# Kernel optimization log

Measured on AMD Instinct MI355X. Metric: run time of the kernel, lower is better.

The kernel has to match this reference:

```python
import jax, jax.numpy as jnp
import numpy as np

B, S_LEN, H, NH, NT, NL, I = 8, 2048, 768, 12, 32, 9, 3072
SPAN = 64
NSP = S_LEN // SPAN
TAG_RATE = 2
DH = H // NH
EPS = 1e-12


def rope(x):
    # interleaved-pair rotary position embedding, x: [B, L, H]
    L = x.shape[1]
    half = x.shape[2] // 2
    inv = 1.0 / (10000.0 ** (jnp.arange(half, dtype=jnp.float32) / half))
    ang = jnp.arange(L, dtype=jnp.float32)[:, None] * inv[None, :]  # [L, half]
    sin, cos = jnp.sin(ang), jnp.cos(ang)
    x2 = x.reshape(x.shape[0], L, half, 2)
    xe, xo = x2[..., 0], x2[..., 1]
    return jnp.stack([xe * cos - xo * sin, xe * sin + xo * cos], axis=-1).reshape(x.shape)


def layernorm(x, g, b):
    m = jnp.mean(x, axis=-1, keepdims=True)
    v = jnp.mean((x - m) ** 2, axis=-1, keepdims=True)
    return (x - m) * jax.lax.rsqrt(v + EPS) * g + b


def mha(q_in, kv_in, Wqkv, bqkv, Wo, bo):
    # torch nn.MultiheadAttention math (eval), batched over leading span axis
    Wq, Wk, Wv = jnp.split(Wqkv, 3, axis=0)
    bq, bk, bv = jnp.split(bqkv, 3)
    def heads(x, W, b):
        return (x @ W.T + b).reshape(x.shape[0], x.shape[1], NH, DH)
    q = heads(q_in, Wq, bq)
    k = heads(kv_in, Wk, bk)
    v = heads(kv_in, Wv, bv)
    scores = jnp.einsum('nqhd,nkhd->nhqk', q, k) * (1.0 / DH ** 0.5)
    a = jax.nn.softmax(scores, axis=-1)
    o = jnp.einsum('nhqk,nkhd->nqhd', a, v).reshape(q_in.shape[0], q_in.shape[1], H)
    return o @ Wo.T + bo


def setup_inputs() -> dict:
    key = jax.random.key(0)
    ks = jax.random.split(key, 16)
    p = lambda i, shape: (0.02 * jax.random.normal(ks[i], shape)).astype(jnp.float32)
    inp = {}
    inp['word_embedding'] = jax.random.normal(ks[0], (B, S_LEN, H), dtype=jnp.float32)
    # fixed-length, non-overlapping spans covering the sequence
    inp['span_starts'] = jnp.broadcast_to(jnp.arange(NSP, dtype=jnp.int32) * SPAN, (B, NSP))
    inp['span_tags'] = jax.random.randint(ks[1], (B, NSP), 0, NT)
    inp['tag_emb'] = p(2, (NT, H))
    inp['sa_Wqkv'] = p(3, (3 * H, H)); inp['sa_bqkv'] = jnp.zeros((3 * H,), jnp.float32)
    inp['sa_Wo'] = p(4, (H, H)); inp['sa_bo'] = jnp.zeros((H,), jnp.float32)
    inp['at_Wqkv'] = p(5, (3 * H, H)); inp['at_bqkv'] = jnp.zeros((3 * H,), jnp.float32)
    inp['at_Wo'] = p(6, (H, H)); inp['at_bo'] = jnp.zeros((H,), jnp.float32)
    inp['an_g'] = jnp.ones((H,), jnp.float32); inp['an_b'] = jnp.zeros((H,), jnp.float32)
    inp['W1'] = p(7, (I, H)); inp['b1'] = jnp.zeros((I,), jnp.float32)
    inp['W2'] = p(8, (H, I)); inp['b2'] = jnp.zeros((H,), jnp.float32)
    inp['fn_g'] = jnp.ones((H,), jnp.float32); inp['fn_b'] = jnp.zeros((H,), jnp.float32)
    inp['Wout'] = p(9, (NL, H)); inp['bout'] = jnp.zeros((NL,), jnp.float32)
    return inp


def reference(word_embedding, span_starts, span_tags, tag_emb,
              sa_Wqkv, sa_bqkv, sa_Wo, sa_bo,
              at_Wqkv, at_bqkv, at_Wo, at_bo,
              an_g, an_b, W1, b1, W2, b2, fn_g, fn_b, Wout, bout):
    raw = word_embedding  # hidden dropout p=0 (eval) -> identity
    xe = rope(word_embedding)
    # pack all spans: [B, NSP*SPAN] token positions
    pos = (span_starts[..., None] + jnp.arange(SPAN)).reshape(B, NSP * SPAN)
    spans = jnp.take_along_axis(xe, pos[..., None], axis=1).reshape(B * NSP, SPAN, H)
    # if_add_a_self_attention: X += self_attention(X, X, X)
    X = spans + mha(spans, spans, sa_Wqkv, sa_bqkv, sa_Wo, sa_bo)
    # enumerate_mode == 'self_attention': prepend tag embedding token, self-attend, drop it
    tagv = tag_emb[span_tags.reshape(-1)][:, None, :]  # [B*NSP, 1, H]
    qkv = jnp.concatenate([tagv, X], axis=1)           # [B*NSP, SPAN+1, H]
    res = mha(qkv, qkv, at_Wqkv, at_bqkv, at_Wo, at_bo)[:, 1:, :]
    # scatter-add results back into the full sequence
    taged = jnp.zeros_like(word_embedding).at[jnp.arange(B)[:, None], pos].add(
        res.reshape(B, NSP * SPAN, H))
    # if_merge_by_add branch
    out_emb = layernorm(raw + taged * TAG_RATE, an_g, an_b)
    ff = jax.nn.relu(out_emb @ W1.T + b1) @ W2.T + b2
    out = layernorm(ff + out_emb, fn_g, fn_b)
    return out @ Wout.T + bout
```

## Files before the change

kernel.cpp:

```cpp
#include <hip/hip_runtime.h>


typedef __attribute__((ext_vector_type(8))) short short8;
typedef __attribute__((ext_vector_type(4))) float f32x4;

typedef const __attribute__((address_space(1))) unsigned int* gas1_t;
typedef __attribute__((address_space(3))) unsigned int* las3_t;

#define DEVI static __device__ __forceinline__

DEVI void gload_lds16(const void* g, void* l){
  __builtin_amdgcn_global_load_lds((gas1_t)g, (las3_t)l, 16, 0, 0);
}

template<int N> DEVI void vmcnt_imm(){
  if constexpr (N == 8) asm volatile("s_waitcnt vmcnt(8)" ::: "memory");
  else if constexpr (N == 4) asm volatile("s_waitcnt vmcnt(4)" ::: "memory");
  else asm volatile("s_waitcnt vmcnt(0)" ::: "memory");
}

DEVI unsigned short f2bf(float f){
  union { float f; unsigned u; } v; v.f = f;
  unsigned u = v.u;
  return (unsigned short)((u + 0x7fffu + ((u >> 16) & 1u)) >> 16);
}
DEVI float bf2f(unsigned short h){
  union { unsigned u; float f; } v; v.u = ((unsigned)h) << 16; return v.f;
}

__global__ void k_ropetab(float2* __restrict__ tab){
  int idx = blockIdx.x * 256 + threadIdx.x;
  if (idx >= 2048 * 384) return;
  int l = idx / 384, i = idx % 384;
  float inv = __expf(-(float)i * (9.210340371976184f / 384.0f));
  float ang = (float)l * inv;
  tab[idx] = make_float2(cosf(ang), sinf(ang));
}

__global__ void k_f2bf_all(const float* __restrict__ s0, const float* __restrict__ s1,
                           const float* __restrict__ s2, const float* __restrict__ s3,
                           const float* __restrict__ s4, const float* __restrict__ s5,
                           unsigned short* __restrict__ dst){
  int i = blockIdx.x * 256 + threadIdx.x;
  int e = i * 4;
  const float* src; int off;
  if      (e < 1769472){ src = s0; off = e; }
  else if (e < 2359296){ src = s1; off = e - 1769472; }
  else if (e < 4128768){ src = s2; off = e - 2359296; }
  else if (e < 4718592){ src = s3; off = e - 4128768; }
  else if (e < 7077888){ src = s4; off = e - 4718592; }
  else                 { src = s5; off = e - 7077888; }
  float4 v = *(const float4*)(src + off);
  ushort4 o;
  o.x = f2bf(v.x); o.y = f2bf(v.y); o.z = f2bf(v.z); o.w = f2bf(v.w);
  *(ushort4*)(dst + e) = o;
}

__global__ void k_gather_rope(const float* __restrict__ we, const int* __restrict__ starts,
                              const float2* __restrict__ tab, unsigned short* __restrict__ spans){
  int idx = blockIdx.x * 256 + threadIdx.x;
  int r  = idx / 192;
  int c4 = idx % 192;
  int span = r >> 6, s = r & 63;
  int b = span >> 5;
  int l = starts[span] + s;
  float4 x = *(const float4*)(we + ((size_t)b * 2048 + l) * 768 + c4 * 4);
  int i0 = c4 * 2;
  float2 cs0 = tab[l * 384 + i0];
  float2 cs1 = tab[l * 384 + i0 + 1];
  ushort4 o;
  o.x = f2bf(x.x * cs0.x - x.y * cs0.y);
  o.y = f2bf(x.x * cs0.y + x.y * cs0.x);
  o.z = f2bf(x.z * cs1.x - x.w * cs1.y);
  o.w = f2bf(x.z * cs1.y + x.w * cs1.x);
  *(ushort4*)(spans + (size_t)r * 768 + c4 * 4) = o;
}

__global__ void k_fill_tag(const float* __restrict__ tag_emb, const int* __restrict__ tags,
                           unsigned short* __restrict__ at_in){
  int span = blockIdx.x;
  int tag = tags[span];
  const float* src = tag_emb + (size_t)tag * 768;
  unsigned short* dst = at_in + (size_t)span * 65 * 768;
  for (int j = threadIdx.x; j < 768; j += 256) dst[j] = f2bf(src[j]);
}

template<int EPI>
__global__ __launch_bounds__(512, 2)
void k_gemm256(const unsigned short* __restrict__ A, const unsigned short* __restrict__ Bw,
               const float* __restrict__ bias, void* __restrict__ outp,
               const unsigned short* __restrict__ resid, int M, int N, int K, int nbx)
{
  __shared__ unsigned short Asl[4 * 256 * 32];
  __shared__ unsigned short Bsl[4 * 256 * 32];
  const int t0 = threadIdx.x;
  const int w = t0 >> 6, lane = t0 & 63;
  const int g = lane >> 4, li = lane & 15;
  const int wm = w >> 2, wn = w & 3;

  const int nwg = gridDim.x;
  const int bid = blockIdx.x;
  const int q = nwg >> 3, r8 = nwg & 7;
  const int xcd = bid & 7, off = bid >> 3;
  const int swz = (xcd < r8 ? xcd * (q + 1) : r8 * (q + 1) + (xcd - r8) * q) + off;
  int mt, nt;
  const int main_ = nbx << 6;
  if (swz >= main_){ mt = 64; nt = swz - main_; }
  else {
    const int s = swz / 12, wv = swz % 12;
    const int nsc = nbx / 3;
    mt = (s / nsc) * 4 + (wv & 3);
    nt = (s % nsc) * 3 + (wv >> 2);
  }
  const int m0 = mt * 256, n0 = nt * 256;

  const int srow = lane >> 2;
  const int sgc = (((lane & 3) ^ ((lane >> 3) & 3)) << 3);
  const int cs = ((g ^ ((li >> 1) & 3)) << 3);

  f32x4 acc[8][4];
  #pragma unroll
  for (int i = 0; i < 8; i++)
    #pragma unroll
    for (int j = 0; j < 4; j++) acc[i][j] = f32x4{0.f, 0.f, 0.f, 0.f};

  const int KT = K >> 5;

  #define STAGE(t_, s_) do { \
    const unsigned short* ga0 = A  + (size_t)(m0 +       w*16 + srow) * K + (t_)*32 + sgc; \
    const unsigned short* ga1 = A  + (size_t)(m0 + 128 + w*16 + srow) * K + (t_)*32 + sgc; \
    const unsigned short* gb0 = Bw + (size_t)(n0 +       w*16 + srow) * K + (t_)*32 + sgc; \
    const unsigned short* gb1 = Bw + (size_t)(n0 + 128 + w*16 + srow) * K + (t_)*32 + sgc; \
    gload_lds16(ga0, Asl + (s_)*8192 + (      w*16)*32); \
    gload_lds16(ga1, Asl + (s_)*8192 + (128 + w*16)*32); \
    gload_lds16(gb0, Bsl + (s_)*8192 + (      w*16)*32); \
    gload_lds16(gb1, Bsl + (s_)*8192 + (128 + w*16)*32); \
  } while(0)

  STAGE(0, 0);
  STAGE(1, 1);
  STAGE(2, 2);
  vmcnt_imm<8>();
  __builtin_amdgcn_s_barrier();

  for (int t = 0; t < KT; ++t){
    const int slot = t & 3;
    const unsigned short* As = Asl + slot * 8192;
    const unsigned short* Bs = Bsl + slot * 8192;

    short8 af[8], bfr[4];
    #pragma unroll
    for (int m = 0; m < 8; m++)
      af[m] = *(const short8*)(As + (wm * 128 + m * 16 + li) * 32 + cs);
    #pragma unroll
    for (int n = 0; n < 4; n++)
      bfr[n] = *(const short8*)(Bs + (wn * 64 + n * 16 + li) * 32 + cs);

    if (t + 3 < KT) STAGE(t + 3, (t + 3) & 3);

    __builtin_amdgcn_s_setprio(1);
    #pragma unroll
    for (int m = 0; m < 8; m++)
      #pragma unroll
      for (int n = 0; n < 4; n++)
        acc[m][n] = __builtin_amdgcn_mfma_f32_16x16x32_bf16(af[m], bfr[n], acc[m][n], 0, 0, 0);
    __builtin_amdgcn_s_setprio(0);

    if (t + 1 < KT){
      __builtin_amdgcn_sched_barrier(0);
      if (t + 3 < KT)      vmcnt_imm<8>();
      else if (t + 2 < KT) vmcnt_imm<4>();
      else                 vmcnt_imm<0>();
      __builtin_amdgcn_s_barrier();
    }
  }
  #undef STAGE

  unsigned short* outb = (unsigned short*)outp;
  float* outf = (float*)outp;
  #pragma unroll
  for (int m = 0; m < 8; m++){
    const int row = m0 + wm * 128 + m * 16 + g * 4;
    #pragma unroll
    for (int n = 0; n < 4; n++){
      const int col = n0 + wn * 64 + n * 16 + li;
      const float bv = bias[col];
      #pragma unroll
      for (int r = 0; r < 4; r++){
        float v = acc[m][n][r] + bv;
        const int orow = row + r;
        if (EPI == 1) v += bf2f(resid[(size_t)orow * N + col]);
        if (EPI == 3) v = v > 0.f ? v : 0.f;
        if (EPI == 2){
          outf[(size_t)orow * N + col] = v;
        } else if (EPI == 1){
          outb[(size_t)(orow + orow / 64 + 1) * N + col] = f2bf(v);
        } else {
          outb[(size_t)orow * N + col] = f2bf(v);
        }
      }
    }
  }
}

template<int AT>
__global__ __launch_bounds__(64)
void k_attn(const unsigned short* __restrict__ qkv, unsigned short* __restrict__ outp)
{
  constexpr int Lkv  = AT ? 65 : 64;
  constexpr int qoff = AT ? 1 : 0;
  constexpr int NKF  = AT ? 5 : 4;
  constexpr int VK   = AT ? 65 : 64;
  constexpr int KKPV = AT ? 3 : 2;
  const int h = blockIdx.x;
  const int span = blockIdx.y;
  const int base = span * Lkv;
  const int lane = threadIdx.x;
  const int g = lane >> 4, li = lane & 15;

  __shared__ unsigned short P[64 * 104];
  if (AT){
    #pragma unroll
    for (int j = 0; j < 16; j++) P[lane * 104 + 80 + j] = 0;
  }

  short8 qf[4][2];
  #pragma unroll
  for (int m = 0; m < 4; m++)
    #pragma unroll
    for (int kq = 0; kq < 2; kq++)
      qf[m][kq] = *(const short8*)(qkv + (size_t)(base + qoff + m * 16 + li) * 2304 + h * 64 + kq * 32 + g * 8);

  f32x4 sc[4][NKF];
  #pragma unroll
  for (int m = 0; m < 4; m++)
    #pragma unroll
    for (int n = 0; n < NKF; n++) sc[m][n] = f32x4{0.f, 0.f, 0.f, 0.f};

  #pragma unroll
  for (int kq = 0; kq < 2; kq++){
    #pragma unroll
    for (int n = 0; n < NKF; n++){
      int krow = n * 16 + li; if (krow >= Lkv) krow = Lkv - 1;
      short8 kf = *(const short8*)(qkv + (size_t)(base + krow) * 2304 + 768 + h * 64 + kq * 32 + g * 8);
      #pragma unroll
      for (int m = 0; m < 4; m++)
        sc[m][n] = __builtin_amdgcn_mfma_f32_16x16x32_bf16(qf[m][kq], kf, sc[m][n], 0, 0, 0);
    }
  }

  const float scale = 0.125f;
  #pragma unroll
  for (int m = 0; m < 4; m++){
    #pragma unroll
    for (int r = 0; r < 4; r++){
      float mx = -1e30f;
      #pragma unroll
      for (int n = 0; n < NKF; n++){
        float v = sc[m][n][r] * scale;
        if (n * 16 + li >= VK) v = -1e30f;
        sc[m][n][r] = v;
        mx = fmaxf(mx, v);
      }
      mx = fmaxf(mx, __shfl_xor(mx, 1, 64));
      mx = fmaxf(mx, __shfl_xor(mx, 2, 64));
      mx = fmaxf(mx, __shfl_xor(mx, 4, 64));
      mx = fmaxf(mx, __shfl_xor(mx, 8, 64));
      float sum = 0.f;
      #pragma unroll
      for (int n = 0; n < NKF; n++){
        float p = __expf(sc[m][n][r] - mx);
        sc[m][n][r] = p;
        sum += p;
      }
      sum += __shfl_xor(sum, 1, 64);
      sum += __shfl_xor(sum, 2, 64);
      sum += __shfl_xor(sum, 4, 64);
      sum += __shfl_xor(sum, 8, 64);
      const float inv = 1.f / sum;
      const int prow = m * 16 + g * 4 + r;
      #pragma unroll
      for (int n = 0; n < NKF; n++)
        P[prow * 104 + n * 16 + li] = f2bf(sc[m][n][r] * inv);
    }
  }
  __syncthreads();

  f32x4 oacc[4][4];
  #pragma unroll
  for (int m = 0; m < 4; m++)
    #pragma unroll
    for (int n = 0; n < 4; n++) oacc[m][n] = f32x4{0.f, 0.f, 0.f, 0.f};

  #pragma unroll
  for (int kp = 0; kp < KKPV; kp++){
    short8 pf[4];
    #pragma unroll
    for (int m = 0; m < 4; m++)
      pf[m] = *(const short8*)(P + (m * 16 + li) * 104 + kp * 32 + g * 8);
    #pragma unroll
    for (int n = 0; n < 4; n++){
      short8 vf;
      #pragma unroll
      for (int i = 0; i < 8; i++){
        int k = kp * 32 + g * 8 + i;
        unsigned short vv = 0;
        if (k < VK) vv = qkv[(size_t)(base + k) * 2304 + 1536 + h * 64 + n * 16 + li];
        vf[i] = (short)vv;
      }
      #pragma unroll
      for (int m = 0; m < 4; m++)
        oacc[m][n] = __builtin_amdgcn_mfma_f32_16x16x32_bf16(pf[m], vf, oacc[m][n], 0, 0, 0);
    }
  }

  #pragma unroll
  for (int m = 0; m < 4; m++)
    #pragma unroll
    for (int n = 0; n < 4; n++)
      #pragma unroll
      for (int r = 0; r < 4; r++){
        int q = m * 16 + g * 4 + r;
        outp[(size_t)(span * 64 + q) * 768 + h * 64 + n * 16 + li] = f2bf(oacc[m][n][r]);
      }
}

__global__ __launch_bounds__(256)
void k_ln1(const float* __restrict__ raw, const float* __restrict__ res,
           const int* __restrict__ starts, const float* __restrict__ gg,
           const float* __restrict__ bb, unsigned short* __restrict__ oe16)
{
  int wave = threadIdx.x >> 6, lane = threadIdx.x & 63;
  int r = blockIdx.x * 4 + wave;
  int span = r >> 6, s = r & 63;
  int b = span >> 5;
  int l = starts[span] + s;
  const float* rp = raw + ((size_t)b * 2048 + l) * 768;
  const float* qp = res + (size_t)r * 768;
  float x[12];
  float sum = 0.f;
  #pragma unroll
  for (int j = 0; j < 12; j++){
    int c = lane + j * 64;
    x[j] = rp[c] + 2.f * qp[c];
    sum += x[j];
  }
  #pragma unroll
  for (int o = 1; o < 64; o <<= 1) sum += __shfl_xor(sum, o, 64);
  float mean = sum * (1.f / 768.f);
  float vs = 0.f;
  #pragma unroll
  for (int j = 0; j < 12; j++){ float d = x[j] - mean; vs += d * d; }
  #pragma unroll
  for (int o = 1; o < 64; o <<= 1) vs += __shfl_xor(vs, o, 64);
  float rstd = rsqrtf(vs * (1.f / 768.f) + 1e-12f);
  size_t ob = ((size_t)b * 2048 + l) * 768;
  #pragma unroll
  for (int j = 0; j < 12; j++){
    int c = lane + j * 64;
    float y = (x[j] - mean) * rstd * gg[c] + bb[c];
    oe16[ob + c] = f2bf(y);
  }
}

__global__ __launch_bounds__(256)
void k_ln2_out(const unsigned short* __restrict__ ff2, const unsigned short* __restrict__ oe,
               const float* __restrict__ gg, const float* __restrict__ bb,
               const float* __restrict__ Wout, const float* __restrict__ bout,
               float* __restrict__ out)
{
  int wave = threadIdx.x >> 6, lane = threadIdx.x & 63;
  int t = blockIdx.x * 4 + wave;
  const unsigned short* fp = ff2 + (size_t)t * 768;
  const unsigned short* ep = oe  + (size_t)t * 768;
  float x[12];
  float sum = 0.f;
  #pragma unroll
  for (int j = 0; j < 12; j++){
    int c = lane + j * 64;
    x[j] = bf2f(fp[c]) + bf2f(ep[c]);
    sum += x[j];
  }
  #pragma unroll
  for (int o = 1; o < 64; o <<= 1) sum += __shfl_xor(sum, o, 64);
  float mean = sum * (1.f / 768.f);
  float vs = 0.f;
  #pragma unroll
  for (int j = 0; j < 12; j++){ float d = x[j] - mean; vs += d * d; }
  #pragma unroll
  for (int o = 1; o < 64; o <<= 1) vs += __shfl_xor(vs, o, 64);
  float rstd = rsqrtf(vs * (1.f / 768.f) + 1e-12f);
  #pragma unroll
  for (int j = 0; j < 12; j++){
    int c = lane + j * 64;
    x[j] = (x[j] - mean) * rstd * gg[c] + bb[c];
  }
  for (int n = 0; n < 9; n++){
    float p = 0.f;
    #pragma unroll
    for (int j = 0; j < 12; j++){
      int c = lane + j * 64;
      p += x[j] * Wout[n * 768 + c];
    }
    #pragma unroll
    for (int o = 1; o < 64; o <<= 1) p += __shfl_xor(p, o, 64);
    if (lane == 0) out[(size_t)t * 9 + n] = p + bout[n];
  }
}

extern "C" void kernel_launch(void* const* d_in, const int* in_sizes, int n_in,
                              void* d_out, int out_size, void* d_ws, size_t ws_size,
                              hipStream_t stream)
{
  const float* we      = (const float*)d_in[0];
  const int*   starts  = (const int*)d_in[1];
  const int*   tags    = (const int*)d_in[2];
  const float* tag_emb = (const float*)d_in[3];
  const float* sa_Wqkv = (const float*)d_in[4];
  const float* sa_bqkv = (const float*)d_in[5];
  const float* sa_Wo   = (const float*)d_in[6];
  const float* sa_bo   = (const float*)d_in[7];
  const float* at_Wqkv = (const float*)d_in[8];
  const float* at_bqkv = (const float*)d_in[9];
  const float* at_Wo   = (const float*)d_in[10];
  const float* at_bo   = (const float*)d_in[11];
  const float* an_g    = (const float*)d_in[12];
  const float* an_b    = (const float*)d_in[13];
  const float* W1      = (const float*)d_in[14];
  const float* b1      = (const float*)d_in[15];
  const float* W2      = (const float*)d_in[16];
  const float* b2      = (const float*)d_in[17];
  const float* fn_g    = (const float*)d_in[18];
  const float* fn_b    = (const float*)d_in[19];
  const float* Wout    = (const float*)d_in[20];
  const float* bout    = (const float*)d_in[21];
  float* out = (float*)d_out;
  char* ws = (char*)d_ws;

  unsigned short* spans   = (unsigned short*)(ws + 0);
  unsigned short* at_in   = (unsigned short*)(ws + 25165824);
  unsigned short* attno   = (unsigned short*)(ws + 50724864);
  unsigned short* qkv     = (unsigned short*)(ws + 75890688);
  float2*         ropetab = (float2*)(ws + 75890688);
  float*          resf    = (float*)(ws + 75890688);
  unsigned short* oe16    = (unsigned short*)(ws + 0);
  unsigned short* ff1     = (unsigned short*)(ws + 25165824);
  unsigned short* ff2     = (unsigned short*)(ws + 125829120);
  unsigned short* wb      = (unsigned short*)(ws + 152567808);
  unsigned short* sa_Wqkv_b = wb;
  unsigned short* sa_Wo_b   = sa_Wqkv_b + 2304 * 768;
  unsigned short* at_Wqkv_b = sa_Wo_b   + 768 * 768;
  unsigned short* at_Wo_b   = at_Wqkv_b + 2304 * 768;
  unsigned short* W1_b      = at_Wo_b   + 768 * 768;
  unsigned short* W2_b      = W1_b      + 3072 * 768;

  k_ropetab<<<3072, 256, 0, stream>>>(ropetab);
  k_f2bf_all<<<9216, 256, 0, stream>>>(sa_Wqkv, sa_Wo, at_Wqkv, at_Wo, W1, W2, wb);
  k_gather_rope<<<12288, 256, 0, stream>>>(we, starts, ropetab, spans);

  k_gemm256<0><<<576, 512, 0, stream>>>(spans, sa_Wqkv_b, sa_bqkv, qkv, nullptr, 16384, 2304, 768, 9);
  k_attn<0><<<dim3(12, 256), 64, 0, stream>>>(qkv, attno);
  k_fill_tag<<<256, 256, 0, stream>>>(tag_emb, tags, at_in);
  k_gemm256<1><<<192, 512, 0, stream>>>(attno, sa_Wo_b, sa_bo, at_in, spans, 16384, 768, 768, 3);
  k_gemm256<0><<<585, 512, 0, stream>>>(at_in, at_Wqkv_b, at_bqkv, qkv, nullptr, 16640, 2304, 768, 9);
  k_attn<1><<<dim3(12, 256), 64, 0, stream>>>(qkv, attno);
  k_gemm256<2><<<192, 512, 0, stream>>>(attno, at_Wo_b, at_bo, resf, nullptr, 16384, 768, 768, 3);
  k_ln1<<<4096, 256, 0, stream>>>(we, resf, starts, an_g, an_b, oe16);
  k_gemm256<3><<<768, 512, 0, stream>>>(oe16, W1_b, b1, ff1, nullptr, 16384, 3072, 768, 12);
  k_gemm256<0><<<192, 512, 0, stream>>>(ff1, W2_b, b2, ff2, nullptr, 16384, 768, 3072, 3);
  k_ln2_out<<<4096, 256, 0, stream>>>(ff2, oe16, fn_g, fn_b, Wout, bout, out);
}
```

Baseline: 500.0 us.

## Split GEMM k-step into two MFMA halves with interleaved A/B staging

The GEMM main loop is unrolled by four so LDS slots are indexed statically. Each k-step is split into two MFMA phases over the upper and lower halves of the A tile. The global-to-LDS loads for A and B are issued separately, one ahead of each phase, with barriers and priority bumps around every phase. The goal is to overlap loads with MFMA work in a finer-grained, ping-pong-like way and to hold fewer A fragments in registers at once. In exchange it adds four barriers per k-step and assumes K/32 is a multiple of four.

```diff
diff --git a/kernel.cpp b/kernel.cpp
--- a/kernel.cpp
+++ b/kernel.cpp
@@ -126,55 +126,72 @@
 
   const int KT = K >> 5;
 
-  #define STAGE(t_, s_) do { \
+  #define STAGE_A(t_, s_) do { \
     const unsigned short* ga0 = A  + (size_t)(m0 +       w*16 + srow) * K + (t_)*32 + sgc; \
     const unsigned short* ga1 = A  + (size_t)(m0 + 128 + w*16 + srow) * K + (t_)*32 + sgc; \
+    gload_lds16(ga0, Asl + (s_)*8192 + (      w*16)*32); \
+    gload_lds16(ga1, Asl + (s_)*8192 + (128 + w*16)*32); \
+  } while(0)
+  #define STAGE_B(t_, s_) do { \
     const unsigned short* gb0 = Bw + (size_t)(n0 +       w*16 + srow) * K + (t_)*32 + sgc; \
     const unsigned short* gb1 = Bw + (size_t)(n0 + 128 + w*16 + srow) * K + (t_)*32 + sgc; \
-    gload_lds16(ga0, Asl + (s_)*8192 + (      w*16)*32); \
-    gload_lds16(ga1, Asl + (s_)*8192 + (128 + w*16)*32); \
     gload_lds16(gb0, Bsl + (s_)*8192 + (      w*16)*32); \
     gload_lds16(gb1, Bsl + (s_)*8192 + (128 + w*16)*32); \
   } while(0)
 
-  STAGE(0, 0);
-  STAGE(1, 1);
-  STAGE(2, 2);
+  STAGE_A(0, 0); STAGE_B(0, 0);
+  STAGE_A(1, 1); STAGE_B(1, 1);
+  STAGE_A(2, 2); STAGE_B(2, 2);
   vmcnt_imm<8>();
   __builtin_amdgcn_s_barrier();
 
-  for (int t = 0; t < KT; ++t){
-    const int slot = t & 3;
-    const unsigned short* As = Asl + slot * 8192;
-    const unsigned short* Bs = Bsl + slot * 8192;
-
-    short8 af[8], bfr[4];
-    #pragma unroll
-    for (int m = 0; m < 8; m++)
-      af[m] = *(const short8*)(As + (wm * 128 + m * 16 + li) * 32 + cs);
-    #pragma unroll
-    for (int n = 0; n < 4; n++)
-      bfr[n] = *(const short8*)(Bs + (wn * 64 + n * 16 + li) * 32 + cs);
-
-    if (t + 3 < KT) STAGE(t + 3, (t + 3) & 3);
-
-    __builtin_amdgcn_s_setprio(1);
-    #pragma unroll
-    for (int m = 0; m < 8; m++)
+  for (int tb = 0; tb < KT; tb += 4){
+    #pragma unroll
+    for (int u = 0; u < 4; u++){
+      const int t = tb + u;
+      const unsigned short* As = Asl + u * 8192;
+      const unsigned short* Bs = Bsl + u * 8192;
+      const int sn = (u + 3) & 3;
+
+      short8 af[4], bfr[4];
+      #pragma unroll
+      for (int m = 0; m < 4; m++)
+        af[m] = *(const short8*)(As + (wm * 128 + m * 16 + li) * 32 + cs);
       #pragma unroll
       for (int n = 0; n < 4; n++)
-        acc[m][n] = __builtin_amdgcn_mfma_f32_16x16x32_bf16(af[m], bfr[n], acc[m][n], 0, 0, 0);
-    __builtin_amdgcn_s_setprio(0);
-
-    if (t + 1 < KT){
-      __builtin_amdgcn_sched_barrier(0);
+        bfr[n] = *(const short8*)(Bs + (wn * 64 + n * 16 + li) * 32 + cs);
+      if (t + 3 < KT) STAGE_A(t + 3, sn);
+      __builtin_amdgcn_s_barrier();
+      __builtin_amdgcn_s_setprio(1);
+      #pragma unroll
+      for (int m = 0; m < 4; m++)
+        #pragma unroll
+        for (int n = 0; n < 4; n++)
+          acc[m][n] = __builtin_amdgcn_mfma_f32_16x16x32_bf16(af[m], bfr[n], acc[m][n], 0, 0, 0);
+      __builtin_amdgcn_s_setprio(0);
+      __builtin_amdgcn_s_barrier();
+
+      short8 af2[4];
+      #pragma unroll
+      for (int m = 0; m < 4; m++)
+        af2[m] = *(const short8*)(As + (wm * 128 + (m + 4) * 16 + li) * 32 + cs);
+      if (t + 3 < KT) STAGE_B(t + 3, sn);
       if (t + 3 < KT)      vmcnt_imm<8>();
       else if (t + 2 < KT) vmcnt_imm<4>();
-      else                 vmcnt_imm<0>();
+      else if (t + 1 < KT) vmcnt_imm<0>();
       __builtin_amdgcn_s_barrier();
-    }
-  }
-  #undef STAGE
+      __builtin_amdgcn_s_setprio(1);
+      #pragma unroll
+      for (int m = 0; m < 4; m++)
+        #pragma unroll
+        for (int n = 0; n < 4; n++)
+          acc[m + 4][n] = __builtin_amdgcn_mfma_f32_16x16x32_bf16(af2[m], bfr[n], acc[m + 4][n], 0, 0, 0);
+      __builtin_amdgcn_s_setprio(0);
+      __builtin_amdgcn_s_barrier();
+    }
+  }
+  #undef STAGE_A
+  #undef STAGE_B
 
   unsigned short* outb = (unsigned short*)outp;
   float* outf = (float*)outp;
```

Result: slower. 532.2 us (+6.5%).
